# Performance work log

Measured on AMD Instinct MI355X. Metric: run time of the kernel, lower is better.

The kernel has to match this reference:

```python
import jax, jax.numpy as jnp
import numpy as np

N = 50000

def sage_conv(x, edge_index, W_l, b_l, W_r):
    # PyG SAGEConv (aggr='mean'): out = lin_l(mean_{j in N(i)} x_j) + lin_r(x_i)
    src, dst = edge_index[0], edge_index[1]
    msg = x[src]                                            # [E, d]
    summed = jax.ops.segment_sum(msg, dst, num_segments=N)  # [N, d]
    deg = jax.ops.segment_sum(jnp.ones((edge_index.shape[1],), x.dtype), dst, num_segments=N)
    agg = summed / jnp.maximum(deg, 1.0)[:, None]
    return agg @ W_l.T + b_l + x @ W_r.T

def setup_inputs() -> dict:
    key = jax.random.key(0)
    ks = jax.random.split(key, 8)
    in_c, hid_c, out_c, E = 128, 256, 128, 800000
    x = jax.random.normal(ks[0], (N, in_c), dtype=jnp.float32)
    edge_index = jax.random.randint(ks[1], (2, E), 0, N, dtype=jnp.int64)
    s = lambda k, shp, fan: jax.random.normal(k, shp, jnp.float32) * (1.0 / np.sqrt(fan))
    return {
        "x": x,
        "edge_index": edge_index,
        "W1_l": s(ks[2], (hid_c, in_c), in_c),
        "b1": jnp.zeros((hid_c,), jnp.float32),
        "W1_r": s(ks[3], (hid_c, in_c), in_c),
        "W2_l": s(ks[4], (out_c, hid_c), hid_c),
        "b2": jnp.zeros((out_c,), jnp.float32),
        "W2_r": s(ks[5], (out_c, hid_c), hid_c),
    }

def reference(x, edge_index, W1_l, b1, W1_r, W2_l, b2, W2_r):
    h = jax.nn.relu(sage_conv(x, edge_index, W1_l, b1, W1_r))
    # dropout is identity in eval mode
    return sage_conv(h, edge_index, W2_l, b2, W2_r)
```

## Files before the change

### kernel.cpp

```cpp
#include <hip/hip_runtime.h>
#include <hip/hip_bf16.h>


typedef short short8 __attribute__((ext_vector_type(8)));
typedef float floatx4 __attribute__((ext_vector_type(4)));

#define IN_C  128
#define HID_C 256
#define OUT_C 128
#define NBMAX 400
#define CHUNK 3072
#define CAP   2560
#define NBIN  261
#define NCAST 200
#define NWPK  56

static __device__ __forceinline__ unsigned short f2b(float f) {
  union { float f; unsigned u; } v; v.f = f;
  unsigned r = v.u + 0x7fffu + ((v.u >> 16) & 1u);
  return (unsigned short)(r >> 16);
}
static __device__ __forceinline__ unsigned pack2(float a, float b) {
  return (unsigned)f2b(a) | ((unsigned)f2b(b) << 16);
}
static __device__ __forceinline__ float lo2f(unsigned u) {
  union { unsigned u; float f; } v; v.u = u << 16; return v.f;
}
static __device__ __forceinline__ float hi2f(unsigned u) {
  union { unsigned u; float f; } v; v.u = u & 0xffff0000u; return v.f;
}


__global__ void __launch_bounds__(512)
k_binprep(const int* __restrict__ ei, int E, int nb,
          int* __restrict__ cursor, unsigned* __restrict__ staged,
          const float* __restrict__ x, unsigned* __restrict__ xb, int nPairsX,
          const float* __restrict__ W1l, const float* __restrict__ W1r,
          const float* __restrict__ W2l, const float* __restrict__ W2r,
          unsigned* __restrict__ wpk1, unsigned* __restrict__ wpk2) {
  __shared__ unsigned sbuf[CHUNK];
  __shared__ int lh[512];
  __shared__ int loff[NBMAX];
  __shared__ int lcnt[NBMAX];
  __shared__ int lcur[NBMAX];
  __shared__ int gb[NBMAX];
  __shared__ int wsum[8];
  int blk = blockIdx.x, tid = threadIdx.x;

  if (blk >= NBIN) {
    if (blk < NBIN + NCAST) {
      for (int i = (blk - NBIN) * 512 + tid; i < nPairsX; i += NCAST * 512) {
        float2 v = reinterpret_cast<const float2*>(x)[i];
        xb[i] = pack2(v.x, v.y);
      }
    } else {
      for (int i = (blk - NBIN - NCAST) * 512 + tid; i < 65536; i += NWPK * 512) {
        if (i < 32768) {
          int r = i >> 7, c = i & 127;
          const float* s = (c < 64) ? (W1l + (size_t)r * 128 + c * 2)
                                    : (W1r + (size_t)r * 128 + (c - 64) * 2);
          float2 v = *reinterpret_cast<const float2*>(s);
          wpk1[i] = pack2(v.x, v.y);
        } else {
          int k = i - 32768;
          const float* s = (k < 16384) ? (W2l + (size_t)k * 2)
                                       : (W2r + (size_t)(k - 16384) * 2);
          float2 v = *reinterpret_cast<const float2*>(s);
          wpk2[k] = pack2(v.x, v.y);
        }
      }
    }
    return;
  }

  int lane = tid & 63, wv = tid >> 6;
  int e0 = blk * CHUNK;
  int e1 = min(e0 + CHUNK, E);
  lh[tid] = 0;
  __syncthreads();
  for (int e = e0 + tid; e < e1; e += 512)
    atomicAdd(&lh[((unsigned)ei[E + e]) >> 7], 1);
  __syncthreads();
  int v = lh[tid];
  int s = v;
#pragma unroll
  for (int off = 1; off < 64; off <<= 1) {
    int t = __shfl_up(s, off, 64);
    if (lane >= off) s += t;
  }
  if (lane == 63) wsum[wv] = s;
  __syncthreads();
  if (wv == 0 && lane < 8) {
    int t = wsum[lane];
#pragma unroll
    for (int off = 1; off < 8; off <<= 1) {
      int u = __shfl_up(t, off, 64);
      if (lane >= off) t += u;
    }
    wsum[lane] = t;
  }
  __syncthreads();
  int woff = (wv == 0) ? 0 : wsum[wv - 1];
  int excl = woff + s - v;
  if (tid < nb) {
    loff[tid] = excl; lcnt[tid] = v; lcur[tid] = excl;
    gb[tid] = tid * CAP + atomicAdd(&cursor[tid], v);
  }
  __syncthreads();
  for (int e = e0 + tid; e < e1; e += 512) {
    int dst = ei[E + e];
    int src = ei[e];
    int b = ((unsigned)dst) >> 7;
    int p = atomicAdd(&lcur[b], 1);
    sbuf[p] = ((unsigned)src << 7) | (unsigned)(dst & 127);
  }
  __syncthreads();
  for (int b = wv; b < nb; b += 8) {
    int lbeg = loff[b], cnt = lcnt[b], gbase = gb[b];
    for (int p = lane; p < cnt; p += 64)
      staged[gbase + p] = sbuf[lbeg + p];
  }
}


__global__ void k_csr(const unsigned* __restrict__ staged, const int* __restrict__ cursor,
                      int2* __restrict__ offs2, int* __restrict__ srcs, int N) {
  __shared__ int cnt[128];
  __shared__ int cur[128];
  int b = blockIdx.x;
  int tid = threadIdx.x;
  int gbeg = b * CAP, gend = gbeg + cursor[b];
  if (tid < 128) cnt[tid] = 0;
  __syncthreads();
  for (int j = gbeg + tid; j < gend; j += 256)
    atomicAdd(&cnt[staged[j] & 127], 1);
  __syncthreads();
  if (tid < 64) {
    int v0 = cnt[tid * 2], v1 = cnt[tid * 2 + 1];
    int s = v0 + v1;
#pragma unroll
    for (int off = 1; off < 64; off <<= 1) {
      int t = __shfl_up(s, off, 64);
      if (tid >= off) s += t;
    }
    int exclp = s - (v0 + v1);
    int node = b * 128 + tid * 2;
    int beg0 = gbeg + exclp;
    int beg1 = beg0 + v0;
    cur[tid * 2]     = beg0;
    cur[tid * 2 + 1] = beg1;
    if (node < N)     offs2[node]     = make_int2(beg0, beg1);
    if (node + 1 < N) offs2[node + 1] = make_int2(beg1, beg1 + v1);
  }
  __syncthreads();
  for (int j = gbeg + tid; j < gend; j += 256) {
    unsigned v = staged[j];
    int pos = atomicAdd(&cur[v & 127], 1);
    srcs[pos] = (int)(v >> 7);
  }
}


static __device__ __forceinline__ void acc8(float* s, uint4 p) {
  s[0] += lo2f(p.x); s[1] += hi2f(p.x);
  s[2] += lo2f(p.y); s[3] += hi2f(p.y);
  s[4] += lo2f(p.z); s[5] += hi2f(p.z);
  s[6] += lo2f(p.w); s[7] += hi2f(p.w);
}

__global__ void k_agg_store(const uint4* __restrict__ Z4,
                            const int2* __restrict__ offs2, const int* __restrict__ srcs,
                            uint4* __restrict__ out4, int N) {
  int node = blockIdx.x * 4 + (threadIdx.x >> 6);
  if (node >= N) return;
  int lane = threadIdx.x & 63;
  int g = lane >> 4, c = lane & 15;
  int2 be = offs2[node];
  int beg = be.x, end = be.y;
  float s[8] = {};
  int j = beg;
  for (; j + 16 <= end; j += 16) {
    uint4 p0 = Z4[(size_t)srcs[j +      g] * 16 + c];
    uint4 p1 = Z4[(size_t)srcs[j +  4 + g] * 16 + c];
    uint4 p2 = Z4[(size_t)srcs[j +  8 + g] * 16 + c];
    uint4 p3 = Z4[(size_t)srcs[j + 12 + g] * 16 + c];
    acc8(s, p0); acc8(s, p1); acc8(s, p2); acc8(s, p3);
  }
  for (; j + 4 <= end; j += 4) {
    uint4 p = Z4[(size_t)srcs[j + g] * 16 + c];
    acc8(s, p);
  }
  if (j + g < end) {
    uint4 p = Z4[(size_t)srcs[j + g] * 16 + c];
    acc8(s, p);
  }
#pragma unroll
  for (int i = 0; i < 8; ++i) {
    s[i] += __shfl_xor(s[i], 16);
    s[i] += __shfl_xor(s[i], 32);
  }
  if (g == 0) {
    int d = end - beg;
    float inv = 1.0f / (float)(d > 0 ? d : 1);
    uint4 o;
    o.x = pack2(s[0] * inv, s[1] * inv);
    o.y = pack2(s[2] * inv, s[3] * inv);
    o.z = pack2(s[4] * inv, s[5] * inv);
    o.w = pack2(s[6] * inv, s[7] * inv);
    out4[(size_t)node * 16 + c] = o;
  }
}

__global__ void k_agg_addout(const uint4* __restrict__ Z4,
                             const int2* __restrict__ offs2, const int* __restrict__ srcs,
                             const uint4* __restrict__ Bb4,
                             float* __restrict__ Out, int N) {
  int node = blockIdx.x * 4 + (threadIdx.x >> 6);
  if (node >= N) return;
  int lane = threadIdx.x & 63;
  int g = lane >> 4, c = lane & 15;
  int2 be = offs2[node];
  int beg = be.x, end = be.y;
  float s[8] = {};
  int j = beg;
  for (; j + 16 <= end; j += 16) {
    uint4 p0 = Z4[(size_t)srcs[j +      g] * 16 + c];
    uint4 p1 = Z4[(size_t)srcs[j +  4 + g] * 16 + c];
    uint4 p2 = Z4[(size_t)srcs[j +  8 + g] * 16 + c];
    uint4 p3 = Z4[(size_t)srcs[j + 12 + g] * 16 + c];
    acc8(s, p0); acc8(s, p1); acc8(s, p2); acc8(s, p3);
  }
  for (; j + 4 <= end; j += 4) {
    uint4 p = Z4[(size_t)srcs[j + g] * 16 + c];
    acc8(s, p);
  }
  if (j + g < end) {
    uint4 p = Z4[(size_t)srcs[j + g] * 16 + c];
    acc8(s, p);
  }
#pragma unroll
  for (int i = 0; i < 8; ++i) {
    s[i] += __shfl_xor(s[i], 16);
    s[i] += __shfl_xor(s[i], 32);
  }
  if (g == 0) {
    int d = end - beg;
    float inv = 1.0f / (float)(d > 0 ? d : 1);
    uint4 bp = Bb4[(size_t)node * 16 + c];
    float4 o0, o1;
    o0.x = lo2f(bp.x) + s[0] * inv; o0.y = hi2f(bp.x) + s[1] * inv;
    o0.z = lo2f(bp.y) + s[2] * inv; o0.w = hi2f(bp.y) + s[3] * inv;
    o1.x = lo2f(bp.z) + s[4] * inv; o1.y = hi2f(bp.z) + s[5] * inv;
    o1.z = lo2f(bp.w) + s[6] * inv; o1.w = hi2f(bp.w) + s[7] * inv;
    float* op = Out + (size_t)node * 128 + c * 8;
    *reinterpret_cast<float4*>(op) = o0;
    *reinterpret_cast<float4*>(op + 4) = o1;
  }
}


static __device__ __forceinline__ void stage_dual(
    const unsigned short* A1, const unsigned short* A2, int mBase,
    unsigned short* At ) {
  int t = threadIdx.x;
#pragma unroll
  for (int it = 0; it < 8; ++it) {
    int q = it * 256 + t;
    int r = q >> 5;
    int p = q & 31;
    int d = (p & 16) | ((p ^ r) & 15);
    const unsigned short* g = (d < 16)
        ? (A1 + (size_t)(mBase + r) * 128 + d * 8)
        : (A2 + (size_t)(mBase + r) * 128 + (d - 16) * 8);
    __builtin_amdgcn_global_load_lds(
        (const __attribute__((address_space(1))) unsigned*)g,
        (__attribute__((address_space(3))) unsigned*)&At[q * 8], 16, 0, 0);
  }
}

static __device__ __forceinline__ void stage_single(
    const unsigned short* A, int mBase, unsigned short* At) {
  int t = threadIdx.x;
#pragma unroll
  for (int it = 0; it < 8; ++it) {
    int q = it * 256 + t;
    int r = q >> 5;
    int p = q & 31;
    int d = (p & 16) | ((p ^ r) & 15);
    const unsigned short* g = A + (size_t)(mBase + r) * 256 + d * 8;
    __builtin_amdgcn_global_load_lds(
        (const __attribute__((address_space(1))) unsigned*)g,
        (__attribute__((address_space(3))) unsigned*)&At[q * 8], 16, 0, 0);
  }
}

__global__ void __launch_bounds__(256, 3)
k_gemm1(const unsigned short* __restrict__ A1, const unsigned short* __restrict__ A2,
        const unsigned short* __restrict__ Wpk, const float* __restrict__ bias,
        unsigned short* __restrict__ H, int M) {
  __shared__ unsigned short At[64 * 256];
  int mBase = blockIdx.x * 64;
  stage_dual(A1, A2, mBase, At);
  int lane = threadIdx.x & 63, wave = threadIdx.x >> 6;
  int l15 = lane & 15, quad = lane >> 4;
  floatx4 acc[4][4] = {};
  __syncthreads();
#pragma unroll 2
  for (int kk = 0; kk < 8; ++kk) {
    int kc = kk * 4 + quad;
    short8 b[4];
#pragma unroll
    for (int t = 0; t < 4; ++t) {
      int n = wave * 64 + t * 16 + l15;
      b[t] = *reinterpret_cast<const short8*>(Wpk + (size_t)n * 256 + kc * 8);
    }
#pragma unroll
    for (int s = 0; s < 4; ++s) {
      int row = s * 16 + l15;
      int pos = (kc & 16) | ((kc ^ row) & 15);
      short8 a = *reinterpret_cast<const short8*>(&At[row * 256 + pos * 8]);
#pragma unroll
      for (int t = 0; t < 4; ++t)
        acc[s][t] = __builtin_amdgcn_mfma_f32_16x16x32_bf16(a, b[t], acc[s][t], 0, 0, 0);
    }
  }
#pragma unroll
  for (int t = 0; t < 4; ++t) {
    int n = wave * 64 + t * 16 + l15;
    float bv = bias[n];
#pragma unroll
    for (int s = 0; s < 4; ++s)
#pragma unroll
      for (int r = 0; r < 4; ++r) {
        int m = mBase + s * 16 + quad * 4 + r;
        if (m < M) H[(size_t)m * 256 + n] = f2b(fmaxf(acc[s][t][r] + bv, 0.f));
      }
  }
}

__global__ void __launch_bounds__(256, 3)
k_gemm2(const unsigned short* __restrict__ H, const unsigned short* __restrict__ Wpk,
        const float* __restrict__ bias, unsigned short* __restrict__ Zb,
        unsigned short* __restrict__ Bb, int M) {
  __shared__ unsigned short At[64 * 256];
  int mBase = blockIdx.x * 64;
  stage_single(H, mBase, At);
  int lane = threadIdx.x & 63, wave = threadIdx.x >> 6;
  int l15 = lane & 15, quad = lane >> 4;
  floatx4 acc[4][4] = {};
  __syncthreads();
#pragma unroll 2
  for (int kk = 0; kk < 8; ++kk) {
    int kc = kk * 4 + quad;
    short8 b[4];
#pragma unroll
    for (int t = 0; t < 4; ++t) {
      int n = wave * 64 + t * 16 + l15;
      b[t] = *reinterpret_cast<const short8*>(Wpk + (size_t)n * 256 + kc * 8);
    }
#pragma unroll
    for (int s = 0; s < 4; ++s) {
      int row = s * 16 + l15;
      int pos = (kc & 16) | ((kc ^ row) & 15);
      short8 a = *reinterpret_cast<const short8*>(&At[row * 256 + pos * 8]);
#pragma unroll
      for (int t = 0; t < 4; ++t)
        acc[s][t] = __builtin_amdgcn_mfma_f32_16x16x32_bf16(a, b[t], acc[s][t], 0, 0, 0);
    }
  }
  if (wave < 2) {
#pragma unroll
    for (int t = 0; t < 4; ++t) {
      int n = wave * 64 + t * 16 + l15;
#pragma unroll
      for (int s = 0; s < 4; ++s)
#pragma unroll
        for (int r = 0; r < 4; ++r) {
          int m = mBase + s * 16 + quad * 4 + r;
          if (m < M) Zb[(size_t)m * 128 + n] = f2b(acc[s][t][r]);
        }
    }
  } else {
#pragma unroll
    for (int t = 0; t < 4; ++t) {
      int n = (wave - 2) * 64 + t * 16 + l15;
      float bv = bias[n];
#pragma unroll
      for (int s = 0; s < 4; ++s)
#pragma unroll
        for (int r = 0; r < 4; ++r) {
          int m = mBase + s * 16 + quad * 4 + r;
          if (m < M) Bb[(size_t)m * 128 + n] = f2b(acc[s][t][r] + bv);
        }
    }
  }
}


extern "C" void kernel_launch(void* const* d_in, const int* in_sizes, int n_in,
                              void* d_out, int out_size, void* d_ws, size_t ws_size,
                              hipStream_t stream) {
  const float* x   = (const float*)d_in[0];
  const int*   ei  = (const int*)d_in[1];
  const float* W1l = (const float*)d_in[2];
  const float* b1  = (const float*)d_in[3];
  const float* W1r = (const float*)d_in[4];
  const float* W2l = (const float*)d_in[5];
  const float* b2  = (const float*)d_in[6];
  const float* W2r = (const float*)d_in[7];
  float* out = (float*)d_out;

  int N = in_sizes[0] / IN_C;
  int E = in_sizes[1] / 2;
  int nb = (N + 127) >> 7;

  char* p = (char*)d_ws;
  auto alloc = [&](size_t bytes) -> void* {
    void* r = (void*)p;
    p += (bytes + 255) & ~(size_t)255;
    return r;
  };
  int* cursor  = (int*)alloc((size_t)(nb + 1) * 4);
  unsigned* staged = (unsigned*)alloc((size_t)nb * CAP * 4);
  int2* offs2 = (int2*)alloc((size_t)N * 8);
  int* srcs   = (int*)alloc((size_t)nb * CAP * 4);
  unsigned* xb   = (unsigned*)alloc((size_t)N * IN_C * 2);
  unsigned* agg1 = (unsigned*)alloc((size_t)N * IN_C * 2);
  unsigned short* hb = (unsigned short*)alloc((size_t)N * HID_C * 2);
  unsigned short* zb = (unsigned short*)alloc((size_t)N * OUT_C * 2);
  unsigned short* baseb = (unsigned short*)alloc((size_t)N * OUT_C * 2);
  unsigned* wpk1 = (unsigned*)alloc((size_t)HID_C * 256 * 2);
  unsigned* wpk2 = (unsigned*)alloc((size_t)256 * HID_C * 2);
  (void)alloc(64 * 512);

  hipMemsetAsync(cursor, 0, (size_t)(nb + 1) * 4, stream);
  k_binprep<<<NBIN + NCAST + NWPK, 512, 0, stream>>>(
      ei, E, nb, cursor, staged, x, xb, N * IN_C / 2,
      W1l, W1r, W2l, W2r, wpk1, wpk2);
  k_csr<<<nb, 256, 0, stream>>>(staged, cursor, offs2, srcs, N);

  int mBlocks = (N + 63) / 64;

  k_agg_store<<<(N + 3) / 4, 256, 0, stream>>>(
      (const uint4*)xb, offs2, srcs, (uint4*)agg1, N);
  k_gemm1<<<mBlocks, 256, 0, stream>>>(
      (const unsigned short*)agg1, (const unsigned short*)xb,
      (const unsigned short*)wpk1, b1, hb, N);

  k_gemm2<<<mBlocks, 256, 0, stream>>>(
      hb, (const unsigned short*)wpk2, b2, zb, baseb, N);
  k_agg_addout<<<(N + 3) / 4, 256, 0, stream>>>(
      (const uint4*)zb, offs2, srcs, (const uint4*)baseb, out, N);
}
```

Measured before the change: 237.4 us.

## Fuse layer-1 and layer-2 GEMMs, keeping hidden activations in LDS

Merges the two GEMM kernels into one. After the first GEMM, each block writes its ReLU'd hidden tile back into the swizzled LDS buffer and runs the second GEMM on it directly. This removes the global round-trip of the N×256 bf16 hidden tensor and one kernel launch. In exchange the kernel holds more accumulator registers, adds barriers, and does scalar LDS stores that may cause bank conflicts.

```diff
diff --git a/kernel.cpp b/kernel.cpp
--- a/kernel.cpp
+++ b/kernel.cpp
@@ -278,31 +278,17 @@
   }
 }
 
-static __device__ __forceinline__ void stage_single(
-    const unsigned short* A, int mBase, unsigned short* At) {
-  int t = threadIdx.x;
-#pragma unroll
-  for (int it = 0; it < 8; ++it) {
-    int q = it * 256 + t;
-    int r = q >> 5;
-    int p = q & 31;
-    int d = (p & 16) | ((p ^ r) & 15);
-    const unsigned short* g = A + (size_t)(mBase + r) * 256 + d * 8;
-    __builtin_amdgcn_global_load_lds(
-        (const __attribute__((address_space(1))) unsigned*)g,
-        (__attribute__((address_space(3))) unsigned*)&At[q * 8], 16, 0, 0);
-  }
-}
-
 __global__ void __launch_bounds__(256, 3)
-k_gemm1(const unsigned short* __restrict__ A1, const unsigned short* __restrict__ A2,
-        const unsigned short* __restrict__ Wpk, const float* __restrict__ bias,
-        unsigned short* __restrict__ H, int M) {
+k_gemm12(const unsigned short* __restrict__ A1, const unsigned short* __restrict__ A2,
+         const unsigned short* __restrict__ Wpk1, const float* __restrict__ b1,
+         const unsigned short* __restrict__ Wpk2, const float* __restrict__ b2,
+         unsigned short* __restrict__ Zb, unsigned short* __restrict__ Bb, int M) {
   __shared__ unsigned short At[64 * 256];
   int mBase = blockIdx.x * 64;
   stage_dual(A1, A2, mBase, At);
   int lane = threadIdx.x & 63, wave = threadIdx.x >> 6;
   int l15 = lane & 15, quad = lane >> 4;
+
   floatx4 acc[4][4] = {};
   __syncthreads();
 #pragma unroll 2
@@ -312,7 +298,7 @@
 #pragma unroll
     for (int t = 0; t < 4; ++t) {
       int n = wave * 64 + t * 16 + l15;
-      b[t] = *reinterpret_cast<const short8*>(Wpk + (size_t)n * 256 + kc * 8);
+      b[t] = *reinterpret_cast<const short8*>(Wpk1 + (size_t)n * 256 + kc * 8);
     }
 #pragma unroll
     for (int s = 0; s < 4; ++s) {
@@ -324,31 +310,26 @@
         acc[s][t] = __builtin_amdgcn_mfma_f32_16x16x32_bf16(a, b[t], acc[s][t], 0, 0, 0);
     }
   }
+  __syncthreads();
+
 #pragma unroll
   for (int t = 0; t < 4; ++t) {
     int n = wave * 64 + t * 16 + l15;
-    float bv = bias[n];
-#pragma unroll
-    for (int s = 0; s < 4; ++s)
+    float bv = b1[n];
+    int d = n >> 3, nl = n & 7;
+#pragma unroll
+    for (int s = 0; s < 4; ++s) {
 #pragma unroll
       for (int r = 0; r < 4; ++r) {
-        int m = mBase + s * 16 + quad * 4 + r;
-        if (m < M) H[(size_t)m * 256 + n] = f2b(fmaxf(acc[s][t][r] + bv, 0.f));
+        int m = s * 16 + quad * 4 + r;
+        int pos = (d & 16) | ((d ^ m) & 15);
+        At[m * 256 + pos * 8 + nl] = f2b(fmaxf(acc[s][t][r] + bv, 0.f));
       }
-  }
-}
-
-__global__ void __launch_bounds__(256, 3)
-k_gemm2(const unsigned short* __restrict__ H, const unsigned short* __restrict__ Wpk,
-        const float* __restrict__ bias, unsigned short* __restrict__ Zb,
-        unsigned short* __restrict__ Bb, int M) {
-  __shared__ unsigned short At[64 * 256];
-  int mBase = blockIdx.x * 64;
-  stage_single(H, mBase, At);
-  int lane = threadIdx.x & 63, wave = threadIdx.x >> 6;
-  int l15 = lane & 15, quad = lane >> 4;
-  floatx4 acc[4][4] = {};
-  __syncthreads();
+    }
+  }
+  __syncthreads();
+
+  floatx4 acc2[4][4] = {};
 #pragma unroll 2
   for (int kk = 0; kk < 8; ++kk) {
     int kc = kk * 4 + quad;
@@ -356,7 +337,7 @@
 #pragma unroll
     for (int t = 0; t < 4; ++t) {
       int n = wave * 64 + t * 16 + l15;
-      b[t] = *reinterpret_cast<const short8*>(Wpk + (size_t)n * 256 + kc * 8);
+      b[t] = *reinterpret_cast<const short8*>(Wpk2 + (size_t)n * 256 + kc * 8);
     }
 #pragma unroll
     for (int s = 0; s < 4; ++s) {
@@ -365,7 +346,7 @@
       short8 a = *reinterpret_cast<const short8*>(&At[row * 256 + pos * 8]);
 #pragma unroll
       for (int t = 0; t < 4; ++t)
-        acc[s][t] = __builtin_amdgcn_mfma_f32_16x16x32_bf16(a, b[t], acc[s][t], 0, 0, 0);
+        acc2[s][t] = __builtin_amdgcn_mfma_f32_16x16x32_bf16(a, b[t], acc2[s][t], 0, 0, 0);
     }
   }
   if (wave < 2) {
@@ -377,20 +358,20 @@
 #pragma unroll
         for (int r = 0; r < 4; ++r) {
           int m = mBase + s * 16 + quad * 4 + r;
-          if (m < M) Zb[(size_t)m * 128 + n] = f2b(acc[s][t][r]);
+          if (m < M) Zb[(size_t)m * 128 + n] = f2b(acc2[s][t][r]);
         }
     }
   } else {
 #pragma unroll
     for (int t = 0; t < 4; ++t) {
       int n = (wave - 2) * 64 + t * 16 + l15;
-      float bv = bias[n];
+      float bv = b2[n];
 #pragma unroll
       for (int s = 0; s < 4; ++s)
 #pragma unroll
         for (int r = 0; r < 4; ++r) {
           int m = mBase + s * 16 + quad * 4 + r;
-          if (m < M) Bb[(size_t)m * 128 + n] = f2b(acc[s][t][r] + bv);
+          if (m < M) Bb[(size_t)m * 128 + n] = f2b(acc2[s][t][r] + bv);
         }
     }
   }
@@ -426,7 +407,6 @@
   int* srcs   = (int*)alloc((size_t)nb * CAP * 4);
   unsigned* xb   = (unsigned*)alloc((size_t)N * IN_C * 2);
   unsigned* agg1 = (unsigned*)alloc((size_t)N * IN_C * 2);
-  unsigned short* hb = (unsigned short*)alloc((size_t)N * HID_C * 2);
   unsigned short* zb = (unsigned short*)alloc((size_t)N * OUT_C * 2);
   unsigned short* baseb = (unsigned short*)alloc((size_t)N * OUT_C * 2);
   unsigned* wpk1 = (unsigned*)alloc((size_t)HID_C * 256 * 2);
@@ -443,12 +423,11 @@
 
   k_agg_store<<<(N + 3) / 4, 256, 0, stream>>>(
       (const uint4*)xb, offs2, srcs, (uint4*)agg1, N);
-  k_gemm1<<<mBlocks, 256, 0, stream>>>(
+  k_gemm12<<<mBlocks, 256, 0, stream>>>(
       (const unsigned short*)agg1, (const unsigned short*)xb,
-      (const unsigned short*)wpk1, b1, hb, N);
-
-  k_gemm2<<<mBlocks, 256, 0, stream>>>(
-      hb, (const unsigned short*)wpk2, b2, zb, baseb, N);
+      (const unsigned short*)wpk1, b1,
+      (const unsigned short*)wpk2, b2, zb, baseb, N);
+
   k_agg_addout<<<(N + 3) / 4, 256, 0, stream>>>(
       (const uint4*)zb, offs2, srcs, (const uint4*)baseb, out, N);
 }
```

Result: faster. 219.6 us (-7.5%).
